# Kernel optimization log

Hardware: AMD Instinct MI355X
Metric: run time of the kernel (lower is better)

The kernel has to match this reference:

```python
import jax, jax.numpy as jnp
import numpy as np

B, L, D, H = 2, 2048, 1024, 16
HD = D // H
SCALE = HD ** (-0.5)


def setup_inputs() -> dict:
    key = jax.random.key(0)
    ks = jax.random.split(key, 12)
    mk = lambda k, shape: (0.02 * jax.random.normal(k, shape, dtype=jnp.float32))
    return {
        "x_real": jax.random.normal(ks[0], (B, L, D), dtype=jnp.float32),
        "x_imag": jax.random.normal(ks[1], (B, L, D), dtype=jnp.float32),
        "wq_r": mk(ks[2], (D, D)),
        "wq_i": mk(ks[3], (D, D)),
        "wk_r": mk(ks[4], (D, D)),
        "wk_i": mk(ks[5], (D, D)),
        "wv_r": mk(ks[6], (D, D)),
        "wv_i": mk(ks[7], (D, D)),
        "wo_r": mk(ks[8], (D, D)),
        "wo_i": mk(ks[9], (D, D)),
        "bo_r": jnp.zeros((D,), dtype=jnp.float32),
        "bo_i": jnp.zeros((D,), dtype=jnp.float32),
    }


def _clinear(xr, xi, wr, wi):
    # (a+bi)(c+di): real = a@Wr^T - b@Wi^T ; imag = a@Wi^T + b@Wr^T
    r = xr @ wr.T - xi @ wi.T
    i = xr @ wi.T + xi @ wr.T
    return r, i


def _heads(t):
    # [B,L,D] -> [B,H,L,hd]
    return t.reshape(B, L, H, HD).transpose(0, 2, 1, 3)


def reference(x_real, x_imag, wq_r, wq_i, wk_r, wk_i, wv_r, wv_i, wo_r, wo_i, bo_r, bo_i):
    Qr, Qi = _clinear(x_real, x_imag, wq_r, wq_i)
    Kr, Ki = _clinear(x_real, x_imag, wk_r, wk_i)
    Vr, Vi = _clinear(x_real, x_imag, wv_r, wv_i)
    Qr, Qi, Kr, Ki, Vr, Vi = map(_heads, (Qr, Qi, Kr, Ki, Vr, Vi))

    # real part of complex dot product: Re(Q)Re(K)^T + Im(Q)Im(K)^T
    scores = (jnp.einsum("bhqd,bhkd->bhqk", Qr, Kr)
              + jnp.einsum("bhqd,bhkd->bhqk", Qi, Ki)) * SCALE
    causal = jnp.tril(jnp.ones((L, L), dtype=bool))
    scores = jnp.where(causal, scores, -jnp.inf)
    w = jax.nn.softmax(scores, axis=-1)

    out_r = jnp.einsum("bhqk,bhkd->bhqd", w, Vr)
    out_i = jnp.einsum("bhqk,bhkd->bhqd", w, Vi)
    merge = lambda t: t.transpose(0, 2, 1, 3).reshape(B, L, D)
    out_r, out_i = merge(out_r), merge(out_i)

    yr, yi = _clinear(out_r, out_i, wo_r, wo_i)
    return yr + bo_r, yi + bo_i
```

## Files before the change

kernel.cpp:

```cpp
#include <hip/hip_runtime.h>
#include <hip/hip_bf16.h>


using f32x4  = __attribute__((ext_vector_type(4))) float;
using short8 = __attribute__((ext_vector_type(8))) short;
using bf16_t = __hip_bfloat16;

#define AS1 __attribute__((address_space(1)))
#define AS3 __attribute__((address_space(3)))

__device__ __forceinline__ void gload_lds16(const bf16_t* g, bf16_t* l) {
  __builtin_amdgcn_global_load_lds((const AS1 unsigned int*)g, (AS3 unsigned int*)l, 16, 0, 0);
}

__device__ __forceinline__ unsigned short bfbits(float f) {
  union { bf16_t h; unsigned short u; } c; c.h = __float2bfloat16(f); return c.u;
}

__global__ void pack_x_k(const float* __restrict__ xr, const float* __restrict__ xi,
                         bf16_t* __restrict__ out) {
  const int total4 = 4096 * 2048 / 4;
  for (int idx = blockIdx.x * blockDim.x + threadIdx.x; idx < total4;
       idx += gridDim.x * blockDim.x) {
    int m = idx >> 9, k = (idx & 511) * 4;
    const float* src = (k < 1024) ? (xr + (size_t)m * 1024 + k)
                                  : (xi + (size_t)m * 1024 + (k - 1024));
    float4 v = *(const float4*)src;
    unsigned int lo = (unsigned)bfbits(v.x) | ((unsigned)bfbits(v.y) << 16);
    unsigned int hi = (unsigned)bfbits(v.z) | ((unsigned)bfbits(v.w) << 16);
    *(uint2*)(out + (size_t)idx * 4) = make_uint2(lo, hi);
  }
}

__global__ void pack_wqkv_k(const float* __restrict__ wqr, const float* __restrict__ wqi,
                            const float* __restrict__ wkr, const float* __restrict__ wki,
                            const float* __restrict__ wvr, const float* __restrict__ wvi,
                            bf16_t* __restrict__ out) {
  const int total4 = 6144 * 2048 / 4;
  for (int idx = blockIdx.x * blockDim.x + threadIdx.x; idx < total4;
       idx += gridDim.x * blockDim.x) {
    int row = idx >> 9, k = (idx & 511) * 4;
    int sec = row >> 10, r1 = row & 1023;
    bool lowk = (k < 1024);
    int kk = lowk ? k : (k - 1024);
    const float* base = wqr; float sg = 1.f;
    switch (sec) {
      case 0: base = lowk ? wqr : wqi; sg = lowk ? 1.f : -1.f; break;
      case 1: base = lowk ? wqi : wqr; break;
      case 2: base = lowk ? wkr : wki; sg = lowk ? 1.f : -1.f; break;
      case 3: base = lowk ? wki : wkr; break;
      case 4: base = lowk ? wvr : wvi; sg = lowk ? 1.f : -1.f; break;
      case 5: base = lowk ? wvi : wvr; break;
    }
    float4 v = *(const float4*)(base + (size_t)r1 * 1024 + kk);
    unsigned int lo = (unsigned)bfbits(v.x * sg) | ((unsigned)bfbits(v.y * sg) << 16);
    unsigned int hi = (unsigned)bfbits(v.z * sg) | ((unsigned)bfbits(v.w * sg) << 16);
    *(uint2*)(out + (size_t)idx * 4) = make_uint2(lo, hi);
  }
}

__global__ void pack_wo_k(const float* __restrict__ wor, const float* __restrict__ woi,
                          bf16_t* __restrict__ out) {
  const int total4 = 2048 * 2048 / 4;
  for (int idx = blockIdx.x * blockDim.x + threadIdx.x; idx < total4;
       idx += gridDim.x * blockDim.x) {
    int row = idx >> 9, k = (idx & 511) * 4;
    int sec = row >> 10, r1 = row & 1023;
    bool lowk = (k < 1024);
    int kk = lowk ? k : (k - 1024);
    const float* base; float sg = 1.f;
    if (sec == 0) { base = lowk ? wor : woi; sg = lowk ? 1.f : -1.f; }
    else          { base = lowk ? woi : wor; }
    float4 v = *(const float4*)(base + (size_t)r1 * 1024 + kk);
    unsigned int lo = (unsigned)bfbits(v.x * sg) | ((unsigned)bfbits(v.y * sg) << 16);
    unsigned int hi = (unsigned)bfbits(v.z * sg) | ((unsigned)bfbits(v.w * sg) << 16);
    *(uint2*)(out + (size_t)idx * 4) = make_uint2(lo, hi);
  }
}

__device__ __forceinline__ void gemm_core(const bf16_t* __restrict__ A,
                                          const bf16_t* __restrict__ W,
                                          int m0, int n0, f32x4 (&acc)[4][4]) {
  __shared__ __align__(16) bf16_t sA[128 * 32];
  __shared__ __align__(16) bf16_t sB[128 * 32];
  const int tid = threadIdx.x;
  const int lane = tid & 63, w = tid >> 6;
  const int wr = w >> 1, wc = w & 1;
  const int quad = lane >> 4, m16 = lane & 15;
  const int c0 = tid, c1 = tid + 256;
  const int r0 = c0 >> 2, o0 = (c0 & 3) * 8;
  const int r1 = c1 >> 2, o1 = (c1 & 3) * 8;
  for (int k0 = 0; k0 < 2048; k0 += 32) {
    __syncthreads();
    gload_lds16(A + (size_t)(m0 + r0) * 2048 + k0 + o0, sA + c0 * 8);
    gload_lds16(A + (size_t)(m0 + r1) * 2048 + k0 + o1, sA + c1 * 8);
    gload_lds16(W + (size_t)(n0 + r0) * 2048 + k0 + o0, sB + c0 * 8);
    gload_lds16(W + (size_t)(n0 + r1) * 2048 + k0 + o1, sB + c1 * 8);
    __syncthreads();
    short8 af[4], bf[4];
#pragma unroll
    for (int i = 0; i < 4; ++i)
      af[i] = *(const short8*)(sA + (wr * 64 + i * 16 + m16) * 32 + quad * 8);
#pragma unroll
    for (int j = 0; j < 4; ++j)
      bf[j] = *(const short8*)(sB + (wc * 64 + j * 16 + m16) * 32 + quad * 8);
#pragma unroll
    for (int i = 0; i < 4; ++i)
#pragma unroll
      for (int j = 0; j < 4; ++j)
        acc[i][j] = __builtin_amdgcn_mfma_f32_16x16x32_bf16(af[i], bf[j], acc[i][j], 0, 0, 0);
  }
}

__global__ __launch_bounds__(256) void gemm_qkv_k(const bf16_t* __restrict__ A,
                                                  const bf16_t* __restrict__ W,
                                                  bf16_t* __restrict__ qk,
                                                  bf16_t* __restrict__ vt) {
  f32x4 acc[4][4] = {};
  const int m0 = blockIdx.x * 128, n0 = blockIdx.y * 128;
  gemm_core(A, W, m0, n0, acc);
  const int lane = threadIdx.x & 63, w = threadIdx.x >> 6;
  const int wr = w >> 1, wc = w & 1, quad = lane >> 4, m16 = lane & 15;
#pragma unroll
  for (int i = 0; i < 4; ++i) {
    const int rowb = m0 + wr * 64 + i * 16 + quad * 4;
#pragma unroll
    for (int j = 0; j < 4; ++j) {
      const int col = n0 + wc * 64 + j * 16 + m16;
      if (col < 4096) {
        const float sc = (col < 2048) ? 0.125f : 1.f;
#pragma unroll
        for (int r = 0; r < 4; ++r)
          qk[(size_t)(rowb + r) * 4096 + col] = __float2bfloat16(acc[i][j][r] * sc);
      } else {
        const int vcol = col - 4096;
        const int ri = vcol >> 10, dfeat = vcol & 1023;
        const int b = rowb >> 11, seq = rowb & 2047;
        const size_t vrow = (size_t)(b * 2048 + (dfeat >> 6) * 128 + ri * 64 + (dfeat & 63));
        unsigned int lo = (unsigned)bfbits(acc[i][j][0]) | ((unsigned)bfbits(acc[i][j][1]) << 16);
        unsigned int hi = (unsigned)bfbits(acc[i][j][2]) | ((unsigned)bfbits(acc[i][j][3]) << 16);
        *(uint2*)(vt + vrow * 2048 + seq) = make_uint2(lo, hi);
      }
    }
  }
}

__global__ __launch_bounds__(256) void gemm_out_k(const bf16_t* __restrict__ A,
                                                  const bf16_t* __restrict__ W,
                                                  const float* __restrict__ bor,
                                                  const float* __restrict__ boi,
                                                  float* __restrict__ out) {
  f32x4 acc[4][4] = {};
  const int m0 = blockIdx.x * 128, n0 = blockIdx.y * 128;
  gemm_core(A, W, m0, n0, acc);
  const int lane = threadIdx.x & 63, w = threadIdx.x >> 6;
  const int wr = w >> 1, wc = w & 1, quad = lane >> 4, m16 = lane & 15;
#pragma unroll
  for (int i = 0; i < 4; ++i) {
    const int rowb = m0 + wr * 64 + i * 16 + quad * 4;
#pragma unroll
    for (int j = 0; j < 4; ++j) {
      const int col = n0 + wc * 64 + j * 16 + m16;
      float bias; float* op;
      if (col < 1024) { bias = bor[col]; op = out + col; }
      else            { bias = boi[col - 1024]; op = out + 4194304 + (col - 1024); }
#pragma unroll
      for (int r = 0; r < 4; ++r)
        op[(size_t)(rowb + r) * 1024] = acc[i][j][r] + bias;
    }
  }
}

__global__ __launch_bounds__(256, 2) void attn_k(const bf16_t* __restrict__ qk,
                                                 const bf16_t* __restrict__ vt,
                                                 bf16_t* __restrict__ acat) {
  __shared__ __align__(16) bf16_t sK[64 * 136];
  __shared__ __align__(16) bf16_t sV[144 * 72];
  __shared__ __align__(16) bf16_t sP[4][2][16 * 72];
  const int tid = threadIdx.x, lane = tid & 63, w = tid >> 6;
  const int quad = lane >> 4, m16 = lane & 15;
  const int x = blockIdx.x, bh = blockIdx.y, b = bh >> 4, h = bh & 15;
  const size_t qkrow0 = (size_t)b * 2048;
  const int qA = x * 64, qB = (31 - x) * 64;
  const int nT = 32 - x;

  {
    const int rr = tid >> 4, cb = (tid & 15) * 4;
    const bf16_t v = __float2bfloat16(rr == 0 ? 1.f : 0.f);
#pragma unroll
    for (int i = 0; i < 4; ++i) sV[(128 + rr) * 72 + cb + i] = v;
  }

  short8 qfA[4], qfB[4];
  {
    const bf16_t* qa = qk + (qkrow0 + qA + w * 16 + m16) * 4096;
    const bf16_t* qb = qk + (qkrow0 + qB + w * 16 + m16) * 4096;
#pragma unroll
    for (int kk = 0; kk < 4; ++kk) {
      const int col = (kk >> 1) * 1024 + h * 64 + (kk & 1) * 32 + quad * 8;
      qfA[kk] = *(const short8*)(qa + col);
      qfB[kk] = *(const short8*)(qb + col);
    }
  }
  f32x4 oA[9], oB[9];
#pragma unroll
  for (int j = 0; j < 9; ++j) { oA[j] = (f32x4){0.f,0.f,0.f,0.f}; oB[j] = (f32x4){0.f,0.f,0.f,0.f}; }

  const int qrowA = qA + w * 16 + quad * 4;
  const int qrowB = qB + w * 16 + quad * 4;

  for (int t = 0; t < nT; ++t) {
    const int k0 = t * 64;
    __syncthreads();
#pragma unroll
    for (int it = 0; it < 4; ++it) {
      const int c = it * 256 + tid;
      const int row = c >> 4, half = (c >> 3) & 1, o8 = (c & 7) * 8;
      *(int4*)(sK + row * 136 + half * 64 + o8) =
          *(const int4*)(qk + (qkrow0 + k0 + row) * 4096 + 2048 + half * 1024 + h * 64 + o8);
    }
#pragma unroll
    for (int it = 0; it < 4; ++it) {
      const int c = it * 256 + tid;
      const int d = c >> 3, k8 = (c & 7) * 8;
      *(int4*)(sV + d * 72 + k8) = *(const int4*)(vt + ((size_t)bh * 128 + d) * 2048 + k0 + k8);
    }
    __syncthreads();

    const bool aAct = (t <= x);
    const bool dgA = (t == x), dgB = (t == nT - 1);

    f32x4 sAv[4], sBv[4];
    if (aAct) {
#pragma unroll
      for (int jt = 0; jt < 4; ++jt) {
        f32x4 a1 = (f32x4){0.f,0.f,0.f,0.f}, a2 = (f32x4){0.f,0.f,0.f,0.f};
#pragma unroll
        for (int kk = 0; kk < 4; ++kk) {
          short8 kf = *(const short8*)(sK + (jt * 16 + m16) * 136 + kk * 32 + quad * 8);
          a1 = __builtin_amdgcn_mfma_f32_16x16x32_bf16(qfA[kk], kf, a1, 0, 0, 0);
          a2 = __builtin_amdgcn_mfma_f32_16x16x32_bf16(qfB[kk], kf, a2, 0, 0, 0);
        }
        sAv[jt] = a1; sBv[jt] = a2;
      }
    } else {
#pragma unroll
      for (int jt = 0; jt < 4; ++jt) {
        f32x4 a2 = (f32x4){0.f,0.f,0.f,0.f};
#pragma unroll
        for (int kk = 0; kk < 4; ++kk) {
          short8 kf = *(const short8*)(sK + (jt * 16 + m16) * 136 + kk * 32 + quad * 8);
          a2 = __builtin_amdgcn_mfma_f32_16x16x32_bf16(qfB[kk], kf, a2, 0, 0, 0);
        }
        sBv[jt] = a2;
      }
    }

    if (aAct) {
      bf16_t* pw = sP[w][0];
#pragma unroll
      for (int jt = 0; jt < 4; ++jt)
#pragma unroll
        for (int r = 0; r < 4; ++r) {
          float s = sAv[jt][r];
          if (dgA && (k0 + jt * 16 + m16 > qrowA + r)) s = -1e30f;
          pw[(quad * 4 + r) * 72 + jt * 16 + m16] = __float2bfloat16(__expf(s));
        }
    }
    {
      bf16_t* pw = sP[w][1];
#pragma unroll
      for (int jt = 0; jt < 4; ++jt)
#pragma unroll
        for (int r = 0; r < 4; ++r) {
          float s = sBv[jt][r];
          if (dgB && (k0 + jt * 16 + m16 > qrowB + r)) s = -1e30f;
          pw[(quad * 4 + r) * 72 + jt * 16 + m16] = __float2bfloat16(__expf(s));
        }
    }
    asm volatile("s_waitcnt lgkmcnt(0)" ::: "memory");

    if (aAct) {
#pragma unroll
      for (int kc = 0; kc < 2; ++kc) {
        short8 pA = *(const short8*)(sP[w][0] + m16 * 72 + kc * 32 + quad * 8);
        short8 pB = *(const short8*)(sP[w][1] + m16 * 72 + kc * 32 + quad * 8);
#pragma unroll
        for (int j = 0; j < 9; ++j) {
          short8 vf = *(const short8*)(sV + (j * 16 + m16) * 72 + kc * 32 + quad * 8);
          oA[j] = __builtin_amdgcn_mfma_f32_16x16x32_bf16(pA, vf, oA[j], 0, 0, 0);
          oB[j] = __builtin_amdgcn_mfma_f32_16x16x32_bf16(pB, vf, oB[j], 0, 0, 0);
        }
      }
    } else {
#pragma unroll
      for (int kc = 0; kc < 2; ++kc) {
        short8 pB = *(const short8*)(sP[w][1] + m16 * 72 + kc * 32 + quad * 8);
#pragma unroll
        for (int j = 0; j < 9; ++j) {
          short8 vf = *(const short8*)(sV + (j * 16 + m16) * 72 + kc * 32 + quad * 8);
          oB[j] = __builtin_amdgcn_mfma_f32_16x16x32_bf16(pB, vf, oB[j], 0, 0, 0);
        }
      }
    }
  }

#pragma unroll
  for (int part = 0; part < 2; ++part) {
    f32x4* o = part ? oB : oA;
    const int qrow = part ? qrowB : qrowA;
    float inv[4];
#pragma unroll
    for (int r = 0; r < 4; ++r)
      inv[r] = 1.f / __shfl(o[8][r], lane & 48);
#pragma unroll
    for (int j = 0; j < 8; ++j) {
      const int d = j * 16 + m16;
      const int col = (d < 64) ? (h * 64 + d) : (1024 + h * 64 + (d - 64));
#pragma unroll
      for (int r = 0; r < 4; ++r)
        acat[((size_t)b * 2048 + qrow + r) * 2048 + col] = __float2bfloat16(o[j][r] * inv[r]);
    }
  }
}

extern "C" void kernel_launch(void* const* d_in, const int* in_sizes, int n_in,
                              void* d_out, int out_size, void* d_ws, size_t ws_size,
                              hipStream_t stream) {
  const float* xr  = (const float*)d_in[0];
  const float* xi  = (const float*)d_in[1];
  const float* wqr = (const float*)d_in[2];
  const float* wqi = (const float*)d_in[3];
  const float* wkr = (const float*)d_in[4];
  const float* wki = (const float*)d_in[5];
  const float* wvr = (const float*)d_in[6];
  const float* wvi = (const float*)d_in[7];
  const float* wor = (const float*)d_in[8];
  const float* woi = (const float*)d_in[9];
  const float* bor = (const float*)d_in[10];
  const float* boi = (const float*)d_in[11];
  float* out = (float*)d_out;

  char* ws = (char*)d_ws;
  bf16_t* Xcat = (bf16_t*)(ws);
  bf16_t* Wqkv = (bf16_t*)(ws + 16777216ull);
  bf16_t* QKb  = (bf16_t*)(ws + 41943040ull);
  bf16_t* Vt   = (bf16_t*)(ws + 75497472ull);
  bf16_t* Acat = (bf16_t*)(ws + 92274688ull);
  bf16_t* Wo   = (bf16_t*)(ws + 109051904ull);

  pack_x_k<<<2048, 256, 0, stream>>>(xr, xi, Xcat);
  pack_wqkv_k<<<2048, 256, 0, stream>>>(wqr, wqi, wkr, wki, wvr, wvi, Wqkv);
  pack_wo_k<<<1024, 256, 0, stream>>>(wor, woi, Wo);
  gemm_qkv_k<<<dim3(32, 48), 256, 0, stream>>>(Xcat, Wqkv, QKb, Vt);
  attn_k<<<dim3(16, 32), 256, 0, stream>>>(QKb, Vt, Acat);
  gemm_out_k<<<dim3(32, 16), 256, 0, stream>>>(Acat, Wo, bor, boi, out);
}
```

Baseline: 404.7 us.

## Swizzle LDS layouts, widen GEMM K-tile, and use direct-to-LDS loads in attention

The GEMM core moves from a K-step of 32 to 64 and stores its A/B tiles in an XOR-swizzled LDS layout, so each barrier pair covers twice the MFMA work and fragment reads avoid bank conflicts without padding. The attention kernel replaces register-staged K and V tile copies with global_load_lds direct-to-LDS transfers, using the same XOR swizzle in place of padded strides. The aim is fewer barriers and VGPR round-trips, plus conflict-free ds_read. The cost is more LDS per GEMM block and swizzled address arithmetic. The ones row at index 128 of sV, used to accumulate the softmax denominator, relies on the new unswizzled writes matching the swizzled reads.

```diff
diff --git a/kernel.cpp b/kernel.cpp
--- a/kernel.cpp
+++ b/kernel.cpp
@@ -81,34 +81,42 @@
 __device__ __forceinline__ void gemm_core(const bf16_t* __restrict__ A,
                                           const bf16_t* __restrict__ W,
                                           int m0, int n0, f32x4 (&acc)[4][4]) {
-  __shared__ __align__(16) bf16_t sA[128 * 32];
-  __shared__ __align__(16) bf16_t sB[128 * 32];
+  __shared__ __align__(16) bf16_t sA[128 * 64];
+  __shared__ __align__(16) bf16_t sB[128 * 64];
   const int tid = threadIdx.x;
   const int lane = tid & 63, w = tid >> 6;
   const int wr = w >> 1, wc = w & 1;
   const int quad = lane >> 4, m16 = lane & 15;
-  const int c0 = tid, c1 = tid + 256;
-  const int r0 = c0 >> 2, o0 = (c0 & 3) * 8;
-  const int r1 = c1 >> 2, o1 = (c1 & 3) * 8;
-  for (int k0 = 0; k0 < 2048; k0 += 32) {
+  const int srow = w * 32 + (lane >> 3);
+  const int gcol = (((lane & 7) ^ (lane >> 3)) * 8);
+  const int swz7 = m16 & 7;
+  for (int k0 = 0; k0 < 2048; k0 += 64) {
     __syncthreads();
-    gload_lds16(A + (size_t)(m0 + r0) * 2048 + k0 + o0, sA + c0 * 8);
-    gload_lds16(A + (size_t)(m0 + r1) * 2048 + k0 + o1, sA + c1 * 8);
-    gload_lds16(W + (size_t)(n0 + r0) * 2048 + k0 + o0, sB + c0 * 8);
-    gload_lds16(W + (size_t)(n0 + r1) * 2048 + k0 + o1, sB + c1 * 8);
+#pragma unroll
+    for (int i = 0; i < 4; ++i) {
+      gload_lds16(A + (size_t)(m0 + srow + i * 8) * 2048 + k0 + gcol,
+                  sA + (size_t)(w * 32 + i * 8) * 64 + lane * 8);
+      gload_lds16(W + (size_t)(n0 + srow + i * 8) * 2048 + k0 + gcol,
+                  sB + (size_t)(w * 32 + i * 8) * 64 + lane * 8);
+    }
     __syncthreads();
-    short8 af[4], bf[4];
-#pragma unroll
-    for (int i = 0; i < 4; ++i)
-      af[i] = *(const short8*)(sA + (wr * 64 + i * 16 + m16) * 32 + quad * 8);
-#pragma unroll
-    for (int j = 0; j < 4; ++j)
-      bf[j] = *(const short8*)(sB + (wc * 64 + j * 16 + m16) * 32 + quad * 8);
-#pragma unroll
-    for (int i = 0; i < 4; ++i)
+#pragma unroll
+    for (int kk = 0; kk < 2; ++kk) {
+      short8 af[4], bf[4];
+#pragma unroll
+      for (int i = 0; i < 4; ++i)
+        af[i] = *(const short8*)(sA + (wr * 64 + i * 16 + m16) * 64 +
+                                 ((kk * 4 + quad) ^ swz7) * 8);
 #pragma unroll
       for (int j = 0; j < 4; ++j)
-        acc[i][j] = __builtin_amdgcn_mfma_f32_16x16x32_bf16(af[i], bf[j], acc[i][j], 0, 0, 0);
+        bf[j] = *(const short8*)(sB + (wc * 64 + j * 16 + m16) * 64 +
+                                 ((kk * 4 + quad) ^ swz7) * 8);
+#pragma unroll
+      for (int i = 0; i < 4; ++i)
+#pragma unroll
+        for (int j = 0; j < 4; ++j)
+          acc[i][j] = __builtin_amdgcn_mfma_f32_16x16x32_bf16(af[i], bf[j], acc[i][j], 0, 0, 0);
+    }
   }
 }
 
@@ -174,8 +182,8 @@
 __global__ __launch_bounds__(256, 2) void attn_k(const bf16_t* __restrict__ qk,
                                                  const bf16_t* __restrict__ vt,
                                                  bf16_t* __restrict__ acat) {
-  __shared__ __align__(16) bf16_t sK[64 * 136];
-  __shared__ __align__(16) bf16_t sV[144 * 72];
+  __shared__ __align__(16) bf16_t sK[64 * 128];
+  __shared__ __align__(16) bf16_t sV[144 * 64];
   __shared__ __align__(16) bf16_t sP[4][2][16 * 72];
   const int tid = threadIdx.x, lane = tid & 63, w = tid >> 6;
   const int quad = lane >> 4, m16 = lane & 15;
@@ -183,12 +191,13 @@
   const size_t qkrow0 = (size_t)b * 2048;
   const int qA = x * 64, qB = (31 - x) * 64;
   const int nT = 32 - x;
+  const int swz7 = m16 & 7;
 
   {
     const int rr = tid >> 4, cb = (tid & 15) * 4;
     const bf16_t v = __float2bfloat16(rr == 0 ? 1.f : 0.f);
 #pragma unroll
-    for (int i = 0; i < 4; ++i) sV[(128 + rr) * 72 + cb + i] = v;
+    for (int i = 0; i < 4; ++i) sV[(128 + rr) * 64 + cb + i] = v;
   }
 
   short8 qfA[4], qfB[4];
@@ -209,21 +218,26 @@
   const int qrowA = qA + w * 16 + quad * 4;
   const int qrowB = qB + w * 16 + quad * 4;
 
+  const int kl4 = lane >> 4, kl15 = lane & 15;
+  const int vl3 = lane >> 3;
+  const int vg7 = ((lane & 7) ^ vl3) * 8;
+
   for (int t = 0; t < nT; ++t) {
     const int k0 = t * 64;
     __syncthreads();
 #pragma unroll
-    for (int it = 0; it < 4; ++it) {
-      const int c = it * 256 + tid;
-      const int row = c >> 4, half = (c >> 3) & 1, o8 = (c & 7) * 8;
-      *(int4*)(sK + row * 136 + half * 64 + o8) =
-          *(const int4*)(qk + (qkrow0 + k0 + row) * 4096 + 2048 + half * 1024 + h * 64 + o8);
-    }
-#pragma unroll
-    for (int it = 0; it < 4; ++it) {
-      const int c = it * 256 + tid;
-      const int d = c >> 3, k8 = (c & 7) * 8;
-      *(int4*)(sV + d * 72 + k8) = *(const int4*)(vt + ((size_t)bh * 128 + d) * 2048 + k0 + k8);
+    for (int i = 0; i < 4; ++i) {
+      const int row = w * 16 + i * 4 + kl4;
+      const int g = kl15 ^ (row & 7);
+      const int col = 2048 + (g >> 3) * 1024 + h * 64 + (g & 7) * 8;
+      gload_lds16(qk + (qkrow0 + k0 + row) * 4096 + col,
+                  sK + (size_t)(w * 16 + i * 4) * 128 + lane * 8);
+    }
+#pragma unroll
+    for (int i = 0; i < 4; ++i) {
+      const int row = w * 32 + i * 8 + vl3;
+      gload_lds16(vt + ((size_t)bh * 128 + row) * 2048 + k0 + vg7,
+                  sV + (size_t)(w * 32 + i * 8) * 64 + lane * 8);
     }
     __syncthreads();
 
@@ -237,7 +251,8 @@
         f32x4 a1 = (f32x4){0.f,0.f,0.f,0.f}, a2 = (f32x4){0.f,0.f,0.f,0.f};
 #pragma unroll
         for (int kk = 0; kk < 4; ++kk) {
-          short8 kf = *(const short8*)(sK + (jt * 16 + m16) * 136 + kk * 32 + quad * 8);
+          short8 kf = *(const short8*)(sK + (jt * 16 + m16) * 128 +
+                                       ((kk * 4 + quad) ^ swz7) * 8);
           a1 = __builtin_amdgcn_mfma_f32_16x16x32_bf16(qfA[kk], kf, a1, 0, 0, 0);
           a2 = __builtin_amdgcn_mfma_f32_16x16x32_bf16(qfB[kk], kf, a2, 0, 0, 0);
         }
@@ -249,7 +264,8 @@
         f32x4 a2 = (f32x4){0.f,0.f,0.f,0.f};
 #pragma unroll
         for (int kk = 0; kk < 4; ++kk) {
-          short8 kf = *(const short8*)(sK + (jt * 16 + m16) * 136 + kk * 32 + quad * 8);
+          short8 kf = *(const short8*)(sK + (jt * 16 + m16) * 128 +
+                                       ((kk * 4 + quad) ^ swz7) * 8);
           a2 = __builtin_amdgcn_mfma_f32_16x16x32_bf16(qfB[kk], kf, a2, 0, 0, 0);
         }
         sBv[jt] = a2;
@@ -287,7 +303,8 @@
         short8 pB = *(const short8*)(sP[w][1] + m16 * 72 + kc * 32 + quad * 8);
 #pragma unroll
         for (int j = 0; j < 9; ++j) {
-          short8 vf = *(const short8*)(sV + (j * 16 + m16) * 72 + kc * 32 + quad * 8);
+          short8 vf = *(const short8*)(sV + (j * 16 + m16) * 64 +
+                                       ((kc * 4 + quad) ^ swz7) * 8);
           oA[j] = __builtin_amdgcn_mfma_f32_16x16x32_bf16(pA, vf, oA[j], 0, 0, 0);
           oB[j] = __builtin_amdgcn_mfma_f32_16x16x32_bf16(pB, vf, oB[j], 0, 0, 0);
         }
@@ -298,7 +315,8 @@
         short8 pB = *(const short8*)(sP[w][1] + m16 * 72 + kc * 32 + quad * 8);
 #pragma unroll
         for (int j = 0; j < 9; ++j) {
-          short8 vf = *(const short8*)(sV + (j * 16 + m16) * 72 + kc * 32 + quad * 8);
+          short8 vf = *(const short8*)(sV + (j * 16 + m16) * 64 +
+                                       ((kc * 4 + quad) ^ swz7) * 8);
           oB[j] = __builtin_amdgcn_mfma_f32_16x16x32_bf16(pB, vf, oB[j], 0, 0, 0);
         }
       }
```

Result: no change. 400.6 us (-1.0%).
